# Performance work log

Hardware: AMD Instinct MI355X
Metric: run time of the kernel (lower is better)

Reference implementation:

```python
import jax, jax.numpy as jnp
from jax import lax
import numpy as np

P = 32      # num_series
H = 128     # hidden units
B = 32      # batch
T = 256     # sequence length

def setup_inputs() -> dict:
    key = jax.random.key(0)
    ks = jax.random.split(key, 8)
    s = 1.0 / np.sqrt(H)
    X     = jax.random.normal(ks[0], (B, T, P), dtype=jnp.float32)
    # per-network LSTM weights, PyTorch gate order (i, f, g, o) stacked in 4H
    W_ih  = jax.random.uniform(ks[1], (P, 4 * H, P), dtype=jnp.float32, minval=-s, maxval=s)
    W_hh  = jax.random.uniform(ks[2], (P, 4 * H, H), dtype=jnp.float32, minval=-s, maxval=s)
    b_ih  = jax.random.uniform(ks[3], (P, 4 * H), dtype=jnp.float32, minval=-s, maxval=s)
    b_hh  = jax.random.uniform(ks[4], (P, 4 * H), dtype=jnp.float32, minval=-s, maxval=s)
    # Conv1d(hidden, 1, kernel_size=1) == per-timestep linear H -> 1, per network
    W_out = jax.random.uniform(ks[5], (P, H), dtype=jnp.float32, minval=-s, maxval=s)
    b_out = jax.random.uniform(ks[6], (P,), dtype=jnp.float32, minval=-s, maxval=s)
    return {"X": X, "W_ih": W_ih, "W_hh": W_hh, "b_ih": b_ih,
            "b_hh": b_hh, "W_out": W_out, "b_out": b_out}

def reference(X, W_ih, W_hh, b_ih, b_hh, W_out, b_out):
    # X: (B, T, P); p independent 1-layer LSTMs run on the same input,
    # batched along a network axis n (size P) with distinct weights.
    # Precompute input projections for all steps/networks: (T, B, P, 4H)
    xproj = jnp.einsum('btd,nkd->tbnk', X, W_ih) + b_ih + b_hh

    def step(carry, xp_t):
        h, c = carry                                   # (B, P, H) each
        gates = xp_t + jnp.einsum('bnh,nkh->bnk', h, W_hh)
        i, f, g, o = jnp.split(gates, 4, axis=-1)
        i = jax.nn.sigmoid(i)
        f = jax.nn.sigmoid(f)
        g = jnp.tanh(g)
        o = jax.nn.sigmoid(o)
        c = f * c + i * g
        h = o * jnp.tanh(c)
        return (h, c), h

    h0 = jnp.zeros((X.shape[0], W_ih.shape[0], W_hh.shape[2]), X.dtype)
    (_, _), hs = lax.scan(step, (h0, h0), xproj)        # hs: (T, B, P, H)
    # 1x1 conv head per network, then concat over networks -> (B, T, P)
    pred = jnp.einsum('tbnh,nh->btn', hs, W_out) + b_out
    return pred
```

## Files before the change

kernel.cpp:

```cpp
#include <hip/hip_runtime.h>
#include <stdint.h>

#define NP 32
#define NH 128
#define NB 32
#define NT 256
#define FH 512

typedef __attribute__((ext_vector_type(4))) float float4_t;
typedef __attribute__((ext_vector_type(8))) __bf16 bf16x8;
typedef __attribute__((ext_vector_type(4))) __bf16 bf16x4;

static __device__ __forceinline__ float4_t mfma_bf16(bf16x8 a, bf16x8 b, float4_t c) {
  return __builtin_amdgcn_mfma_f32_16x16x32_bf16(a, b, c, 0, 0, 0);
}

#define LOG2E 1.4426950408889634f

#define BAR() __asm__ volatile("s_waitcnt lgkmcnt(0)\n\ts_barrier" ::: "memory")
#define SB()  __builtin_amdgcn_sched_barrier(0)


__global__ __launch_bounds__(512, 1) void xcvt(
    const float* __restrict__ X, __bf16* __restrict__ Xb)
{
  const int i = (blockIdx.x * 512 + threadIdx.x) * 4;
  float4_t v = *(const float4_t*)(X + i);
  bf16x4 o;
#pragma unroll
  for (int j = 0; j < 4; ++j) o[j] = (__bf16)v[j];
  *(bf16x4*)(Xb + i) = o;
}

__global__ __attribute__((amdgpu_flat_work_group_size(512, 512),
                          amdgpu_waves_per_eu(2, 2)))
void clstm_fused4(
    const __bf16* __restrict__ Xb, const float* __restrict__ Wih,
    const float* __restrict__ Whh, const float* __restrict__ bih,
    const float* __restrict__ bhh, const float* __restrict__ Wout,
    const float* __restrict__ bout, float* __restrict__ out)
{
  const int net = blockIdx.x >> 3, bq = blockIdx.x & 7;
  const int tid = threadIdx.x;
  const int w = tid >> 6, lane = tid & 63;
  const int quad = lane >> 4, l16 = lane & 15;

  __shared__ __bf16 hfrag[2][4][4][4][8];

  { ((int*)hfrag)[tid] = 0; }
  __syncthreads();

  bf16x8 bfrag[4][5];
  float4_t bias4[4];
#pragma unroll
  for (int g = 0; g < 4; ++g) {
    const float scale = (g == 2) ? (-2.0f*LOG2E) : (-LOG2E);
    const int col = g*NH + w*16 + l16;
#pragma unroll
    for (int kc = 0; kc < 5; ++kc) {
      const float* src = (kc == 0) ? (Wih + ((size_t)net*FH + col)*NP + quad*8)
                                   : (Whh + ((size_t)net*FH + col)*NH + (kc-1)*32 + quad*8);
      bf16x8 bf;
#pragma unroll
      for (int j = 0; j < 8; ++j) bf[j] = (__bf16)(src[j] * scale);
      bfrag[g][kc] = bf;
    }
    const float b = (bih[net*FH + col] + bhh[net*FH + col]) * scale;
    bias4[g] = (float4_t){b, b, b, b};
  }

  bf16x8 wof[4];
#pragma unroll
  for (int kc = 0; kc < 4; ++kc) {
    const float* wp = Wout + net*NH + kc*32 + quad*8;
#pragma unroll
    for (int j = 0; j < 8; ++j) wof[kc][j] = (__bf16)wp[j];
  }
  const float bo = bout[net];

  float cs = 0.f;
  const float S2 = -2.0f*LOG2E;

  int xoff = (bq*4 + (l16 & 3))*(NT*NP) + quad*8;

  const int kcp = w >> 1, q2 = ((w & 1) << 1) | (l16 >> 3), jj = l16 & 7;

  float* outp = out + ((size_t)bq*4)*(NT*NP) + net;

  bf16x8 ax = *(const bf16x8*)(Xb + xoff);
  xoff += NP;

#define STEP(RD, WR, T_)                                                      \
  do {                                                                        \
       \
    bf16x8 ah0 = *(const bf16x8*)&hfrag[RD][0][quad][l16 & 3][0];             \
    bf16x8 ah1 = *(const bf16x8*)&hfrag[RD][1][quad][l16 & 3][0];             \
    bf16x8 ah2 = *(const bf16x8*)&hfrag[RD][2][quad][l16 & 3][0];             \
    bf16x8 ah3 = *(const bf16x8*)&hfrag[RD][3][quad][l16 & 3][0];             \
    float4_t a0 = mfma_bf16(ax, bfrag[0][0], bias4[0]);                       \
    float4_t a1 = mfma_bf16(ax, bfrag[1][0], bias4[1]);                       \
    float4_t a2 = mfma_bf16(ax, bfrag[2][0], bias4[2]);                       \
    float4_t a3 = mfma_bf16(ax, bfrag[3][0], bias4[3]);                       \
    if ((T_) + 1 < NT) ax = *(const bf16x8*)(Xb + xoff);                      \
    xoff += NP;                                                               \
    a0 = mfma_bf16(ah0, bfrag[0][1], a0);                                     \
    a1 = mfma_bf16(ah0, bfrag[1][1], a1);                                     \
    a0 = mfma_bf16(ah1, bfrag[0][2], a0);                                     \
    a1 = mfma_bf16(ah1, bfrag[1][2], a1);                                     \
    a0 = mfma_bf16(ah2, bfrag[0][3], a0);                                     \
    a1 = mfma_bf16(ah2, bfrag[1][3], a1);                                     \
    a0 = mfma_bf16(ah3, bfrag[0][4], a0);                                     \
    a1 = mfma_bf16(ah3, bfrag[1][4], a1);                                     \
    SB();                                                                     \
          \
    float gi = (quad & 2) ? ((quad & 1) ? a0[3] : a0[2])                      \
                          : ((quad & 1) ? a0[1] : a0[0]);                     \
    float gf = (quad & 2) ? ((quad & 1) ? a1[3] : a1[2])                      \
                          : ((quad & 1) ? a1[1] : a1[0]);                     \
    float ei = __builtin_amdgcn_exp2f(gi);                                    \
    float ig = __builtin_amdgcn_rcpf(1.0f + ei);                              \
    float ef = __builtin_amdgcn_exp2f(gf);                                    \
    float fg = __builtin_amdgcn_rcpf(1.0f + ef);                              \
    SB();                                                                     \
                                                     \
    a2 = mfma_bf16(ah0, bfrag[2][1], a2);                                     \
    a3 = mfma_bf16(ah0, bfrag[3][1], a3);                                     \
    a2 = mfma_bf16(ah1, bfrag[2][2], a2);                                     \
    a3 = mfma_bf16(ah1, bfrag[3][2], a3);                                     \
    a2 = mfma_bf16(ah2, bfrag[2][3], a2);                                     \
    a3 = mfma_bf16(ah2, bfrag[3][3], a3);                                     \
    a2 = mfma_bf16(ah3, bfrag[2][4], a2);                                     \
    a3 = mfma_bf16(ah3, bfrag[3][4], a3);                                     \
    SB();                                                                     \
                          \
    float gg = (quad & 2) ? ((quad & 1) ? a2[3] : a2[2])                      \
                          : ((quad & 1) ? a2[1] : a2[0]);                     \
    float go = (quad & 2) ? ((quad & 1) ? a3[3] : a3[2])                      \
                          : ((quad & 1) ? a3[1] : a3[0]);                     \
    float eg = __builtin_amdgcn_exp2f(fminf(gg, 126.0f));                     \
    float rg = __builtin_amdgcn_rcpf(1.0f + eg);                              \
    float t0 = S2 * rg;                                                       \
    float gg2 = t0 - t0 * eg;                                 \
    float eo = __builtin_amdgcn_exp2f(go);                                    \
    float og = __builtin_amdgcn_rcpf(1.0f + eo);                              \
    cs = fg * cs + ig * gg2;                                      \
    float ec = __builtin_amdgcn_exp2f(fminf(cs, 126.0f));                     \
    float rc = __builtin_amdgcn_rcpf(1.0f + ec);                              \
    float h_ = og * (rc - ec * rc);                          \
    hfrag[WR][kcp][q2][quad][jj] = (__bf16)h_;                                \
    if ((T_) > 0 && w == ((T_) & 7)) {                                        \
      float4_t p0 = {bo, bo, bo, bo};                                         \
      float4_t p1 = {0.f, 0.f, 0.f, 0.f};                                     \
      p0 = mfma_bf16(ah0, wof[0], p0);                                        \
      p1 = mfma_bf16(ah2, wof[2], p1);                                        \
      p0 = mfma_bf16(ah1, wof[1], p0);                                        \
      p1 = mfma_bf16(ah3, wof[3], p1);                                        \
      float4_t po = p0 + p1;                                                  \
      if (lane == 0) {                                                        \
        _Pragma("unroll")                                                     \
        for (int r = 0; r < 4; ++r)                                           \
          outp[(size_t)r*(NT*NP) + ((T_) - 1)*NP] = po[r];                    \
      }                                                                       \
    }                                                                         \
    BAR();                                                                    \
  } while (0)

  for (int t = 0; t < NT; t += 2) {
    STEP(0, 1, t);
    STEP(1, 0, t + 1);
  }
#undef STEP

  if (w == 0) {
    bf16x8 ahf[4];
#pragma unroll
    for (int kc = 0; kc < 4; ++kc)
      ahf[kc] = *(const bf16x8*)&hfrag[NT & 1][kc][quad][l16 & 3][0];
    float4_t p0 = {bo, bo, bo, bo};
    float4_t p1 = {0.f, 0.f, 0.f, 0.f};
    p0 = mfma_bf16(ahf[0], wof[0], p0);
    p1 = mfma_bf16(ahf[2], wof[2], p1);
    p0 = mfma_bf16(ahf[1], wof[1], p0);
    p1 = mfma_bf16(ahf[3], wof[3], p1);
    float4_t po = p0 + p1;
    if (lane == 0) {
#pragma unroll
      for (int r = 0; r < 4; ++r)
        outp[(size_t)r*(NT*NP) + (NT - 1)*NP] = po[r];
    }
  }
}

__global__ __launch_bounds__(512, 1) void clstm_fused_fb(
    const float* __restrict__ X, const float* __restrict__ Wih,
    const float* __restrict__ Whh, const float* __restrict__ bih,
    const float* __restrict__ bhh, const float* __restrict__ Wout,
    const float* __restrict__ bout, float* __restrict__ out)
{
  const int net = blockIdx.x >> 3, bq = blockIdx.x & 7;
  const int tid = threadIdx.x;
  const int w = tid >> 6, lane = tid & 63;
  const int quad = lane >> 4, l16 = lane & 15;

  __shared__ __bf16 hfrag[2][4][4][4][8];
  { ((int*)hfrag)[tid] = 0; }
  __syncthreads();

  bf16x8 bfrag[4][5];
  float4_t bias4[4];
#pragma unroll
  for (int g = 0; g < 4; ++g) {
    const float scale = (g == 2) ? (-2.0f*LOG2E) : (-LOG2E);
    const int col = g*NH + w*16 + l16;
#pragma unroll
    for (int kc = 0; kc < 5; ++kc) {
      const float* src = (kc == 0) ? (Wih + ((size_t)net*FH + col)*NP + quad*8)
                                   : (Whh + ((size_t)net*FH + col)*NH + (kc-1)*32 + quad*8);
      bf16x8 bf;
#pragma unroll
      for (int j = 0; j < 8; ++j) bf[j] = (__bf16)(src[j] * scale);
      bfrag[g][kc] = bf;
    }
    const float b = (bih[net*FH + col] + bhh[net*FH + col]) * scale;
    bias4[g] = (float4_t){b, b, b, b};
  }

  bf16x8 wof[4];
#pragma unroll
  for (int kc = 0; kc < 4; ++kc) {
    const float* wp = Wout + net*NH + kc*32 + quad*8;
#pragma unroll
    for (int j = 0; j < 8; ++j) wof[kc][j] = (__bf16)wp[j];
  }
  const float bo = bout[net];

  float cs = 0.f;
  const float S2 = -2.0f*LOG2E;

  const float* xrow = X + (size_t)(bq*4 + (l16 & 3))*(NT*NP) + quad*8;
  const int kcp = w >> 1, q2 = ((w & 1) << 1) | (l16 >> 3), jj = l16 & 7;
  float* outp = out + ((size_t)bq*4)*(NT*NP) + net;

  bf16x8 ax;
  {
    float xv0[8];
    *(float4_t*)&xv0[0] = *(const float4_t*)xrow;
    *(float4_t*)&xv0[4] = *(const float4_t*)(xrow + 4);
#pragma unroll
    for (int j = 0; j < 8; ++j) ax[j] = (__bf16)xv0[j];
  }
  const float* xp = xrow + NP;
  float xv[8] = {0.f,0.f,0.f,0.f,0.f,0.f,0.f,0.f};

  for (int t = 0; t < NT; ++t) {
    const int rd = t & 1, wr = rd ^ 1;
    bf16x8 ah[4];
#pragma unroll
    for (int kc = 0; kc < 4; ++kc)
      ah[kc] = *(const bf16x8*)&hfrag[rd][kc][quad][l16 & 3][0];
    float4_t accx[4];
#pragma unroll
    for (int g = 0; g < 4; ++g)
      accx[g] = mfma_bf16(ax, bfrag[g][0], bias4[g]);
    if (t + 1 < NT) {
      *(float4_t*)&xv[0] = *(const float4_t*)xp;
      *(float4_t*)&xv[4] = *(const float4_t*)(xp + 4);
    }
    float4_t acc[4];
#pragma unroll
    for (int g = 0; g < 4; ++g) {
      float4_t a0 = mfma_bf16(ah[0], bfrag[g][1], accx[g]);
      float4_t a1 = mfma_bf16(ah[2], bfrag[g][3], (float4_t){0.f,0.f,0.f,0.f});
      a0 = mfma_bf16(ah[1], bfrag[g][2], a0);
      a1 = mfma_bf16(ah[3], bfrag[g][4], a1);
      acc[g] = a0 + a1;
    }
    float gv[4];
#pragma unroll
    for (int g = 0; g < 4; ++g) {
      float a01 = (quad & 1) ? acc[g][1] : acc[g][0];
      float a23 = (quad & 1) ? acc[g][3] : acc[g][2];
      gv[g] = (quad & 2) ? a23 : a01;
    }
    float h;
    {
      float ei = __builtin_amdgcn_exp2f(gv[0]);
      float ig = __builtin_amdgcn_rcpf(1.0f + ei);
      float ef = __builtin_amdgcn_exp2f(gv[1]);
      float fg = __builtin_amdgcn_rcpf(1.0f + ef);
      float eg = __builtin_amdgcn_exp2f(fminf(gv[2], 126.0f));
      float rg = __builtin_amdgcn_rcpf(1.0f + eg);
      float t0 = S2 * rg;
      float gg2 = t0 - t0 * eg;
      float eo = __builtin_amdgcn_exp2f(gv[3]);
      float og = __builtin_amdgcn_rcpf(1.0f + eo);
      cs = fg * cs + ig * gg2;
      float ec = __builtin_amdgcn_exp2f(fminf(cs, 126.0f));
      float rc = __builtin_amdgcn_rcpf(1.0f + ec);
      float th = rc - ec * rc;
      h = og * th;
    }
    hfrag[wr][kcp][q2][quad][jj] = (__bf16)h;
    if (w == 0 && t > 0) {
      float4_t p0 = {bo, bo, bo, bo};
      float4_t p1 = {0.f, 0.f, 0.f, 0.f};
      p0 = mfma_bf16(ah[0], wof[0], p0);
      p1 = mfma_bf16(ah[2], wof[2], p1);
      p0 = mfma_bf16(ah[1], wof[1], p0);
      p1 = mfma_bf16(ah[3], wof[3], p1);
      float4_t po = p0 + p1;
      if (lane == 0) {
#pragma unroll
        for (int r = 0; r < 4; ++r)
          outp[(size_t)r*(NT*NP) + (t - 1)*NP] = po[r];
      }
    }
#pragma unroll
    for (int j = 0; j < 8; ++j) ax[j] = (__bf16)xv[j];
    xp += NP;
    BAR();
  }

  if (w == 0) {
    bf16x8 ahf[4];
#pragma unroll
    for (int kc = 0; kc < 4; ++kc)
      ahf[kc] = *(const bf16x8*)&hfrag[NT & 1][kc][quad][l16 & 3][0];
    float4_t p0 = {bo, bo, bo, bo};
    float4_t p1 = {0.f, 0.f, 0.f, 0.f};
    p0 = mfma_bf16(ahf[0], wof[0], p0);
    p1 = mfma_bf16(ahf[2], wof[2], p1);
    p0 = mfma_bf16(ahf[1], wof[1], p0);
    p1 = mfma_bf16(ahf[3], wof[3], p1);
    float4_t po = p0 + p1;
    if (lane == 0) {
#pragma unroll
      for (int r = 0; r < 4; ++r)
        outp[(size_t)r*(NT*NP) + (NT - 1)*NP] = po[r];
    }
  }
}

extern "C" void kernel_launch(void* const* d_in, const int* in_sizes, int n_in,
                              void* d_out, int out_size, void* d_ws, size_t ws_size,
                              hipStream_t stream) {
  const float* X    = (const float*)d_in[0];
  const float* Wih  = (const float*)d_in[1];
  const float* Whh  = (const float*)d_in[2];
  const float* bih  = (const float*)d_in[3];
  const float* bhh  = (const float*)d_in[4];
  const float* Wout = (const float*)d_in[5];
  const float* bout = (const float*)d_in[6];
  float* out = (float*)d_out;
  (void)in_sizes; (void)n_in; (void)out_size;

  const size_t need = (size_t)NB*NT*NP*2;
  if (d_ws != nullptr && ws_size >= need) {
    __bf16* wsX = (__bf16*)d_ws;
    xcvt<<<128, 512, 0, stream>>>(X, wsX);
    clstm_fused4<<<256, 512, 0, stream>>>(wsX, Wih, Whh, bih, bhh, Wout,
                                          bout, out);
  } else {
    clstm_fused_fb<<<256, 512, 0, stream>>>(X, Wih, Whh, bih, bhh, Wout,
                                            bout, out);
  }
}
```

Baseline: 220.3 us.

## Hoist next-step input MFMA before barrier and drop per-quad gate select

Issues the x-projection MFMAs for the next timestep at the end of the current step, so they run ahead of the barrier and leave the critical path. The A-operand rows are remapped (l16>>2 instead of l16&3) so each lane's gate value sits in element 0 of the accumulator, which removes the quad-dependent select chains. The scheduling barriers that split the i/f and g/o phases are gone, so all 16 recurrent MFMAs issue back-to-back. Block-to-(net,batch) mapping is changed and the output store becomes one store per quad instead of lane 0 writing four values.

```diff
diff --git a/kernel.cpp b/kernel.cpp
--- a/kernel.cpp
+++ b/kernel.cpp
@@ -18,7 +18,6 @@
 #define LOG2E 1.4426950408889634f
 
 #define BAR() __asm__ volatile("s_waitcnt lgkmcnt(0)\n\ts_barrier" ::: "memory")
-#define SB()  __builtin_amdgcn_sched_barrier(0)
 
 
 __global__ __launch_bounds__(512, 1) void xcvt(
@@ -34,13 +33,13 @@
 
 __global__ __attribute__((amdgpu_flat_work_group_size(512, 512),
                           amdgpu_waves_per_eu(2, 2)))
-void clstm_fused4(
+void clstm_fused6(
     const __bf16* __restrict__ Xb, const float* __restrict__ Wih,
     const float* __restrict__ Whh, const float* __restrict__ bih,
     const float* __restrict__ bhh, const float* __restrict__ Wout,
     const float* __restrict__ bout, float* __restrict__ out)
 {
-  const int net = blockIdx.x >> 3, bq = blockIdx.x & 7;
+  const int net = blockIdx.x & 31, bq = blockIdx.x >> 5;
   const int tid = threadIdx.x;
   const int w = tid >> 6, lane = tid & 63;
   const int quad = lane >> 4, l16 = lane & 15;
@@ -81,73 +80,65 @@
   float cs = 0.f;
   const float S2 = -2.0f*LOG2E;
 
-  int xoff = (bq*4 + (l16 & 3))*(NT*NP) + quad*8;
+  int xoff = (bq*4 + (l16 >> 2))*(NT*NP) + quad*8;
 
   const int kcp = w >> 1, q2 = ((w & 1) << 1) | (l16 >> 3), jj = l16 & 7;
 
-  float* outp = out + ((size_t)bq*4)*(NT*NP) + net;
+  float* outp = out + ((size_t)(bq*4 + quad))*(NT*NP) + net;
 
   bf16x8 ax = *(const bf16x8*)(Xb + xoff);
   xoff += NP;
+  float4_t a0 = mfma_bf16(ax, bfrag[0][0], bias4[0]);
+  float4_t a1 = mfma_bf16(ax, bfrag[1][0], bias4[1]);
+  float4_t a2 = mfma_bf16(ax, bfrag[2][0], bias4[2]);
+  float4_t a3 = mfma_bf16(ax, bfrag[3][0], bias4[3]);
 
 #define STEP(RD, WR, T_)                                                      \
   do {                                                                        \
-       \
-    bf16x8 ah0 = *(const bf16x8*)&hfrag[RD][0][quad][l16 & 3][0];             \
-    bf16x8 ah1 = *(const bf16x8*)&hfrag[RD][1][quad][l16 & 3][0];             \
-    bf16x8 ah2 = *(const bf16x8*)&hfrag[RD][2][quad][l16 & 3][0];             \
-    bf16x8 ah3 = *(const bf16x8*)&hfrag[RD][3][quad][l16 & 3][0];             \
-    float4_t a0 = mfma_bf16(ax, bfrag[0][0], bias4[0]);                       \
-    float4_t a1 = mfma_bf16(ax, bfrag[1][0], bias4[1]);                       \
-    float4_t a2 = mfma_bf16(ax, bfrag[2][0], bias4[2]);                       \
-    float4_t a3 = mfma_bf16(ax, bfrag[3][0], bias4[3]);                       \
-    if ((T_) + 1 < NT) ax = *(const bf16x8*)(Xb + xoff);                      \
-    xoff += NP;                                                               \
+                 \
+    bf16x8 ah0 = *(const bf16x8*)&hfrag[RD][0][quad][l16 >> 2][0];            \
+    bf16x8 ah1 = *(const bf16x8*)&hfrag[RD][1][quad][l16 >> 2][0];            \
+    bf16x8 ah2 = *(const bf16x8*)&hfrag[RD][2][quad][l16 >> 2][0];            \
+    bf16x8 ah3 = *(const bf16x8*)&hfrag[RD][3][quad][l16 >> 2][0];            \
+        \
     a0 = mfma_bf16(ah0, bfrag[0][1], a0);                                     \
     a1 = mfma_bf16(ah0, bfrag[1][1], a1);                                     \
+    a2 = mfma_bf16(ah0, bfrag[2][1], a2);                                     \
+    a3 = mfma_bf16(ah0, bfrag[3][1], a3);                                     \
     a0 = mfma_bf16(ah1, bfrag[0][2], a0);                                     \
     a1 = mfma_bf16(ah1, bfrag[1][2], a1);                                     \
+    a2 = mfma_bf16(ah1, bfrag[2][2], a2);                                     \
+    a3 = mfma_bf16(ah1, bfrag[3][2], a3);                                     \
     a0 = mfma_bf16(ah2, bfrag[0][3], a0);                                     \
     a1 = mfma_bf16(ah2, bfrag[1][3], a1);                                     \
+    a2 = mfma_bf16(ah2, bfrag[2][3], a2);                                     \
+    a3 = mfma_bf16(ah2, bfrag[3][3], a3);                                     \
     a0 = mfma_bf16(ah3, bfrag[0][4], a0);                                     \
     a1 = mfma_bf16(ah3, bfrag[1][4], a1);                                     \
-    SB();                                                                     \
-          \
-    float gi = (quad & 2) ? ((quad & 1) ? a0[3] : a0[2])                      \
-                          : ((quad & 1) ? a0[1] : a0[0]);                     \
-    float gf = (quad & 2) ? ((quad & 1) ? a1[3] : a1[2])                      \
-                          : ((quad & 1) ? a1[1] : a1[0]);                     \
-    float ei = __builtin_amdgcn_exp2f(gi);                                    \
-    float ig = __builtin_amdgcn_rcpf(1.0f + ei);                              \
-    float ef = __builtin_amdgcn_exp2f(gf);                                    \
-    float fg = __builtin_amdgcn_rcpf(1.0f + ef);                              \
-    SB();                                                                     \
-                                                     \
-    a2 = mfma_bf16(ah0, bfrag[2][1], a2);                                     \
-    a3 = mfma_bf16(ah0, bfrag[3][1], a3);                                     \
-    a2 = mfma_bf16(ah1, bfrag[2][2], a2);                                     \
-    a3 = mfma_bf16(ah1, bfrag[3][2], a3);                                     \
-    a2 = mfma_bf16(ah2, bfrag[2][3], a2);                                     \
-    a3 = mfma_bf16(ah2, bfrag[3][3], a3);                                     \
     a2 = mfma_bf16(ah3, bfrag[2][4], a2);                                     \
     a3 = mfma_bf16(ah3, bfrag[3][4], a3);                                     \
-    SB();                                                                     \
-                          \
-    float gg = (quad & 2) ? ((quad & 1) ? a2[3] : a2[2])                      \
-                          : ((quad & 1) ? a2[1] : a2[0]);                     \
-    float go = (quad & 2) ? ((quad & 1) ? a3[3] : a3[2])                      \
-                          : ((quad & 1) ? a3[1] : a3[0]);                     \
-    float eg = __builtin_amdgcn_exp2f(fminf(gg, 126.0f));                     \
+      \
+    if ((T_) + 1 < NT)                                                        \
+      ax = *(const bf16x8*)(Xb + xoff);                                       \
+    xoff += NP;                                                               \
+                \
+    float ei = __builtin_amdgcn_exp2f(a0[0]);                                 \
+    float ig = __builtin_amdgcn_rcpf(1.0f + ei);              \
+    float ef = __builtin_amdgcn_exp2f(a1[0]);                                 \
+    float fg = __builtin_amdgcn_rcpf(1.0f + ef);              \
+    float eg = __builtin_amdgcn_exp2f(fminf(a2[0], 126.0f));                  \
     float rg = __builtin_amdgcn_rcpf(1.0f + eg);                              \
     float t0 = S2 * rg;                                                       \
     float gg2 = t0 - t0 * eg;                                 \
-    float eo = __builtin_amdgcn_exp2f(go);                                    \
-    float og = __builtin_amdgcn_rcpf(1.0f + eo);                              \
+    float eo = __builtin_amdgcn_exp2f(a3[0]);                                 \
+    float og = __builtin_amdgcn_rcpf(1.0f + eo);              \
     cs = fg * cs + ig * gg2;                                      \
     float ec = __builtin_amdgcn_exp2f(fminf(cs, 126.0f));                     \
     float rc = __builtin_amdgcn_rcpf(1.0f + ec);                              \
-    float h_ = og * (rc - ec * rc);                          \
+    float h_ = og * (rc - ec * rc);                            \
+                       \
     hfrag[WR][kcp][q2][quad][jj] = (__bf16)h_;                                \
+          \
     if ((T_) > 0 && w == ((T_) & 7)) {                                        \
       float4_t p0 = {bo, bo, bo, bo};                                         \
       float4_t p1 = {0.f, 0.f, 0.f, 0.f};                                     \
@@ -155,13 +146,14 @@
       p1 = mfma_bf16(ah2, wof[2], p1);                                        \
       p0 = mfma_bf16(ah1, wof[1], p0);                                        \
       p1 = mfma_bf16(ah3, wof[3], p1);                                        \
-      float4_t po = p0 + p1;                                                  \
-      if (lane == 0) {                                                        \
-        _Pragma("unroll")                                                     \
-        for (int r = 0; r < 4; ++r)                                           \
-          outp[(size_t)r*(NT*NP) + ((T_) - 1)*NP] = po[r];                    \
-      }                                                                       \
+      if (l16 == 0)                                                           \
+        outp[(size_t)((T_) - 1)*NP] = p0[0] + p1[0];                          \
     }                                                                         \
+           \
+    a0 = mfma_bf16(ax, bfrag[0][0], bias4[0]);                                \
+    a1 = mfma_bf16(ax, bfrag[1][0], bias4[1]);                                \
+    a2 = mfma_bf16(ax, bfrag[2][0], bias4[2]);                                \
+    a3 = mfma_bf16(ax, bfrag[3][0], bias4[3]);                                \
     BAR();                                                                    \
   } while (0)
 
@@ -175,19 +167,15 @@
     bf16x8 ahf[4];
 #pragma unroll
     for (int kc = 0; kc < 4; ++kc)
-      ahf[kc] = *(const bf16x8*)&hfrag[NT & 1][kc][quad][l16 & 3][0];
+      ahf[kc] = *(const bf16x8*)&hfrag[NT & 1][kc][quad][l16 >> 2][0];
     float4_t p0 = {bo, bo, bo, bo};
     float4_t p1 = {0.f, 0.f, 0.f, 0.f};
     p0 = mfma_bf16(ahf[0], wof[0], p0);
     p1 = mfma_bf16(ahf[2], wof[2], p1);
     p0 = mfma_bf16(ahf[1], wof[1], p0);
     p1 = mfma_bf16(ahf[3], wof[3], p1);
-    float4_t po = p0 + p1;
-    if (lane == 0) {
-#pragma unroll
-      for (int r = 0; r < 4; ++r)
-        outp[(size_t)r*(NT*NP) + (NT - 1)*NP] = po[r];
-    }
+    if (l16 == 0)
+      outp[(size_t)(NT - 1)*NP] = p0[0] + p1[0];
   }
 }
 
@@ -358,7 +346,7 @@
   if (d_ws != nullptr && ws_size >= need) {
     __bf16* wsX = (__bf16*)d_ws;
     xcvt<<<128, 512, 0, stream>>>(X, wsX);
-    clstm_fused4<<<256, 512, 0, stream>>>(wsX, Wih, Whh, bih, bhh, Wout,
+    clstm_fused6<<<256, 512, 0, stream>>>(wsX, Wih, Whh, bih, bhh, Wout,
                                           bout, out);
   } else {
     clstm_fused_fb<<<256, 512, 0, stream>>>(X, Wih, Whh, bih, bhh, Wout,
```

Result: faster. 213.1 us (-3.3%).
